# Kernel tuning notes

Measured on AMD Instinct MI355X. Metric: run time of the kernel, lower is better.

## Reference

```python
import jax, jax.numpy as jnp
import numpy as np

TOP_K = 12
OBS_RADIUS = 1.0
DIST_MIN_THRES = 0.8
EPS = 1e-4


def setup_inputs() -> dict:
    key = jax.random.key(0)
    ks = jax.random.split(key, 9)
    N, in_dim = 4096, 4
    c = in_dim + 2  # pairwise diff + eye flag + (dist - thres)
    states = jax.random.normal(ks[0], (N, in_dim), dtype=jnp.float32) * 2.0
    def w(k, o, i):
        return jax.random.normal(k, (o, i), dtype=jnp.float32) * (1.0 / np.sqrt(i))
    return {
        "states": states,
        "W1": w(ks[1], 64, c),  "b1": jnp.zeros((64,), jnp.float32),
        "W2": w(ks[2], 128, 64), "b2": jnp.zeros((128,), jnp.float32),
        "W3": w(ks[3], 64, 128), "b3": jnp.zeros((64,), jnp.float32),
        "W4": w(ks[4], 1, 64),   "b4": jnp.zeros((1,), jnp.float32),
    }


def _conv1x1(h, W, b):
    # h: [N, C_in, L]; 1x1 Conv1d == channel matmul
    return jnp.einsum('oi,nil->nol', W, h) + b[None, :, None]


def reference(states, W1, b1, W2, b2, W3, b3, W4, b4):
    N = states.shape[0]
    # pairwise differences: [N, N, in_dim]
    x = states[:, None, :] - states[None, :, :]
    d_norm = jnp.sqrt(jnp.sum(jnp.square(x[:, :, :2]) + EPS, axis=2))  # [N, N]
    eye = jnp.eye(N, dtype=x.dtype)
    x = jnp.concatenate(
        [x, eye[:, :, None], (d_norm - DIST_MIN_THRES)[:, :, None]], axis=2
    )  # [N, N, c]
    # remove_distant_agents: keep TOP_K nearest neighbors per agent
    dn = jnp.sqrt(jnp.sum(jnp.square(x[:, :, :2]) + EPS, axis=2))  # [N, N]
    _, idx = jax.lax.top_k(-dn, TOP_K)                              # [N, k]
    x = jnp.take_along_axis(x, idx[:, :, None], axis=1)            # [N, k, c]
    dist = jnp.sqrt(jnp.sum(jnp.square(x[:, :, :2]) + EPS, axis=2, keepdims=True))  # [N,k,1]
    k, c = x.shape[1], x.shape[2]
    mask = (dist <= OBS_RADIUS).astype(x.dtype).reshape(-1, 1, k)  # [N,1,k] (reshape, as in source)
    h = x.reshape(-1, c, k)  # faithful: source uses reshape, NOT transpose
    h = jax.nn.relu(_conv1x1(h, W1, b1))
    h = jax.nn.relu(_conv1x1(h, W2, b2))
    h = jax.nn.relu(_conv1x1(h, W3, b3))
    h = _conv1x1(h, W4, b4)  # [N, 1, k]
    h = h * mask
    return h, mask
```

## Files before the change

kernel.cpp:

```cpp
#include <hip/hip_runtime.h>
#include <stdint.h>

#define NAG 4096
#define TOPK 12
#define EPSF 1e-4f
#define NT 256
#define PT (NAG / NT)
#define MTOT (NAG * TOPK)

typedef unsigned long long u64;
typedef short short8v __attribute__((ext_vector_type(8)));
typedef float f32x4 __attribute__((ext_vector_type(4)));

__device__ __forceinline__ u64 umin64(u64 a, u64 b) { return a < b ? a : b; }

__device__ __forceinline__ unsigned short f2bf(float f) {
    union { float f; unsigned u; } v; v.f = f;
    unsigned r = v.u + 0x7FFFu + ((v.u >> 16) & 1u);
    return (unsigned short)(r >> 16);
}

template <int CTRL>
__device__ __forceinline__ void dpp_min_step(unsigned &hi, unsigned &lo) {
    unsigned ohi = (unsigned)__builtin_amdgcn_update_dpp((int)hi, (int)hi, CTRL, 0xf, 0xf, false);
    unsigned olo = (unsigned)__builtin_amdgcn_update_dpp((int)lo, (int)lo, CTRL, 0xf, 0xf, false);
    bool t = (ohi < hi) || (ohi == hi && olo < lo);
    hi = t ? ohi : hi;
    lo = t ? olo : lo;
}

__global__ __launch_bounds__(NT, 8)
void cbf_select(const float* __restrict__ states,
                float* __restrict__ xbuf,
                float* __restrict__ out)
{
    const int i = blockIdx.x;
    const int t = threadIdx.x;
    const int lane = t & 63;
    const int wv = t >> 6;

    __shared__ u64 s_min[NT];
    __shared__ u64 s_surv[128];
    __shared__ int s_sel[TOPK];
    __shared__ float s_x[72];
    __shared__ unsigned s_cnt;
    __shared__ unsigned s_T;

    if (t == 0) s_cnt = 0;

    const float2* st2 = reinterpret_cast<const float2*>(states);
    const float si0 = states[i * 4 + 0];
    const float si1 = states[i * 4 + 1];

    unsigned dnb[PT];
    float mind = 1e30f;
    int minu = 0;
#pragma unroll
    for (int u = 0; u < PT; ++u) {
        int j = u * NT + t;
        float2 sj = st2[j * 2];
        float dx0 = __fsub_rn(si0, sj.x);
        float dx1 = __fsub_rn(si1, sj.y);
        float d2 = __fadd_rn(__fadd_rn(__fmul_rn(dx0, dx0), EPSF),
                             __fadd_rn(__fmul_rn(dx1, dx1), EPSF));
        float dn = __fsqrt_rn(d2);
        dnb[u] = __float_as_uint(dn);
        if (dn < mind) { mind = dn; minu = u; }
    }
    s_min[t] = ((u64)__float_as_uint(mind) << 32) | (unsigned)(minu * NT + t);
    __syncthreads();

    if (wv == 0) {
        unsigned khi[4], klo[4];
#pragma unroll
        for (int q = 0; q < 4; ++q) {
            u64 kk = s_min[lane + q * 64];
            klo[q] = (unsigned)(kk & 0xffffffffull);
            khi[q] = (unsigned)(kk >> 32);
        }
        unsigned Tb = 0;
        for (int r = 0; r < TOPK; ++r) {
            unsigned hi = khi[0], lo = klo[0];
#pragma unroll
            for (int q = 1; q < 4; ++q) {
                bool tk = (khi[q] < hi) || (khi[q] == hi && klo[q] < lo);
                hi = tk ? khi[q] : hi;
                lo = tk ? klo[q] : lo;
            }
            dpp_min_step<0xB1>(hi, lo);
            dpp_min_step<0x4E>(hi, lo);
            dpp_min_step<0x124>(hi, lo);
            dpp_min_step<0x128>(hi, lo);
            dpp_min_step<0x142>(hi, lo);
            dpp_min_step<0x143>(hi, lo);
            unsigned hw = (unsigned)__builtin_amdgcn_readlane((int)hi, 63);
            unsigned lw = (unsigned)__builtin_amdgcn_readlane((int)lo, 63);
            Tb = hw;
#pragma unroll
            for (int q = 0; q < 4; ++q) {
                bool w = (khi[q] == hw) && (klo[q] == lw);
                khi[q] = w ? 0xFFFFFFFFu : khi[q];
            }
        }
        if (lane == 0) s_T = Tb;
    }
    __syncthreads();

    {
        unsigned Tb = s_T;
#pragma unroll
        for (int u = 0; u < PT; ++u) {
            if (dnb[u] <= Tb) {
                unsigned slot = atomicAdd(&s_cnt, 1u);
                if (slot < 128)
                    s_surv[slot] = ((u64)dnb[u] << 32) | (unsigned)(u * NT + t);
            }
        }
    }
    __syncthreads();

    if (wv == 0) {
        int cnt = (int)s_cnt;
        if (cnt > 128) cnt = 128;
        u64 kA = (lane < cnt) ? s_surv[lane] : ~0ull;
        u64 kB = (lane + 64 < cnt) ? s_surv[lane + 64] : ~0ull;
        int rA = 0, rB = 0;
        for (int q = 0; q < cnt; ++q) {
            u64 kq = s_surv[q];
            rA += (kq < kA) ? 1 : 0;
            rB += (kq < kB) ? 1 : 0;
        }
        if (lane < cnt && rA < TOPK) s_sel[rA] = (int)(unsigned)(kA & 0xffffffffull);
        if (lane + 64 < cnt && rB < TOPK) s_sel[rB] = (int)(unsigned)(kB & 0xffffffffull);
    }
    __syncthreads();

    if (t < TOPK) {
        int j = s_sel[t];
        const float4 sj = reinterpret_cast<const float4*>(states)[j];
        const float4 si = reinterpret_cast<const float4*>(states)[i];
        float dx0 = __fsub_rn(si.x, sj.x);
        float dx1 = __fsub_rn(si.y, sj.y);
        float dx2 = __fsub_rn(si.z, sj.z);
        float dx3 = __fsub_rn(si.w, sj.w);
        float d2 = __fadd_rn(__fadd_rn(__fmul_rn(dx0, dx0), EPSF),
                             __fadd_rn(__fmul_rn(dx1, dx1), EPSF));
        float dn = __fsqrt_rn(d2);
        s_x[t * 6 + 0] = dx0;
        s_x[t * 6 + 1] = dx1;
        s_x[t * 6 + 2] = dx2;
        s_x[t * 6 + 3] = dx3;
        s_x[t * 6 + 4] = (j == i) ? 1.0f : 0.0f;
        s_x[t * 6 + 5] = __fsub_rn(dn, 0.8f);
        out[MTOT + i * TOPK + t] = (dn <= 1.0f) ? 1.0f : 0.0f;
    }
    __syncthreads();

    if (t < TOPK) {
        int m = i * TOPK + t;
        float4 v0 = {s_x[0 * 12 + t], s_x[1 * 12 + t], s_x[2 * 12 + t], s_x[3 * 12 + t]};
        float4 v1 = {s_x[4 * 12 + t], s_x[5 * 12 + t], 0.0f, 0.0f};
        reinterpret_cast<float4*>(xbuf + m * 8)[0] = v0;
        reinterpret_cast<float4*>(xbuf + m * 8)[1] = v1;
    }
}

__global__ __launch_bounds__(256)
void cbf_mlp(const float* __restrict__ xbuf,
             const float* __restrict__ W1, const float* __restrict__ b1,
             const float* __restrict__ W2, const float* __restrict__ b2,
             const float* __restrict__ W3, const float* __restrict__ b3,
             const float* __restrict__ W4, const float* __restrict__ b4,
             float* __restrict__ out)
{
    const int t = threadIdx.x;
    const int lane = t & 63;
    const int wv = t >> 6;
    const int r16 = lane & 15;
    const int hi = lane >> 4;
    const int m0 = blockIdx.x * 64 + wv * 16;

    __shared__ __align__(16) unsigned char s_h1[4 * 2048];
    __shared__ __align__(16) unsigned char s_h2[4 * 4096];
    unsigned char* lp1 = s_h1 + wv * 2048;
    unsigned char* lp2 = s_h2 + wv * 4096;

    const int mrow = m0 + r16;
    const float4 xa = reinterpret_cast<const float4*>(xbuf + mrow * 8)[0];
    const float4 xb = reinterpret_cast<const float4*>(xbuf + mrow * 8)[1];
    const float xc[6] = {xa.x, xa.y, xa.z, xa.w, xb.x, xb.y};

    unsigned short h1b[16];
#pragma unroll
    for (int ol = 0; ol < 16; ++ol) {
        int o = hi * 16 + ol;
        const float2* wr = reinterpret_cast<const float2*>(W1 + o * 6);
        float2 w0 = wr[0], w1 = wr[1], w2 = wr[2];
        float acc = b1[o];
        acc = fmaf(w0.x, xc[0], acc);
        acc = fmaf(w0.y, xc[1], acc);
        acc = fmaf(w1.x, xc[2], acc);
        acc = fmaf(w1.y, xc[3], acc);
        acc = fmaf(w2.x, xc[4], acc);
        acc = fmaf(w2.y, xc[5], acc);
        h1b[ol] = f2bf(fmaxf(acc, 0.0f));
    }
    {
        short8v p0, p1;
#pragma unroll
        for (int e = 0; e < 8; ++e) { p0[e] = (short)h1b[e]; p1[e] = (short)h1b[8 + e]; }
        int rowb = r16 * 128;
        *(short8v*)(lp1 + rowb + (((2 * hi + 0) ^ (r16 & 7)) * 16)) = p0;
        *(short8v*)(lp1 + rowb + (((2 * hi + 1) ^ (r16 & 7)) * 16)) = p1;
    }
    __syncthreads();

    short8v a0 = *(short8v*)(lp1 + r16 * 128 + (((0 + hi) ^ (r16 & 7)) * 16));
    short8v a1 = *(short8v*)(lp1 + r16 * 128 + (((4 + hi) ^ (r16 & 7)) * 16));
    const int c = r16;
#pragma unroll
    for (int nt = 0; nt < 8; ++nt) {
        const float* wrow = W2 + (nt * 16 + c) * 64;
        float4 g0 = *(const float4*)(wrow + 8 * hi);
        float4 g1 = *(const float4*)(wrow + 8 * hi + 4);
        float4 g2 = *(const float4*)(wrow + 32 + 8 * hi);
        float4 g3 = *(const float4*)(wrow + 36 + 8 * hi);
        short8v bf0, bf1;
        bf0[0] = (short)f2bf(g0.x); bf0[1] = (short)f2bf(g0.y);
        bf0[2] = (short)f2bf(g0.z); bf0[3] = (short)f2bf(g0.w);
        bf0[4] = (short)f2bf(g1.x); bf0[5] = (short)f2bf(g1.y);
        bf0[6] = (short)f2bf(g1.z); bf0[7] = (short)f2bf(g1.w);
        bf1[0] = (short)f2bf(g2.x); bf1[1] = (short)f2bf(g2.y);
        bf1[2] = (short)f2bf(g2.z); bf1[3] = (short)f2bf(g2.w);
        bf1[4] = (short)f2bf(g3.x); bf1[5] = (short)f2bf(g3.y);
        bf1[6] = (short)f2bf(g3.z); bf1[7] = (short)f2bf(g3.w);
        float bb = b2[nt * 16 + c];
        f32x4 acc = {bb, bb, bb, bb};
        acc = __builtin_amdgcn_mfma_f32_16x16x32_bf16(a0, bf0, acc, 0, 0, 0);
        acc = __builtin_amdgcn_mfma_f32_16x16x32_bf16(a1, bf1, acc, 0, 0, 0);
#pragma unroll
        for (int e = 0; e < 4; ++e) {
            unsigned short hv = f2bf(fmaxf(acc[e], 0.0f));
            int mr = 4 * hi + e;
            int slot = (2 * nt + (c >> 3)) ^ (mr & 15);
            *(unsigned short*)(lp2 + mr * 256 + slot * 16 + ((2 * c) & 15)) = hv;
        }
    }
    __syncthreads();

    short8v a3[4];
#pragma unroll
    for (int ks = 0; ks < 4; ++ks)
        a3[ks] = *(short8v*)(lp2 + r16 * 256 + (((4 * ks + hi) ^ r16) * 16));
    float h3r[4][4];
#pragma unroll
    for (int nt = 0; nt < 4; ++nt) {
        const float* wrow = W3 + (nt * 16 + c) * 128;
        float bb = b3[nt * 16 + c];
        f32x4 ac = {bb, bb, bb, bb};
#pragma unroll
        for (int ks = 0; ks < 4; ++ks) {
            float4 q0 = *(const float4*)(wrow + ks * 32 + 8 * hi);
            float4 q1 = *(const float4*)(wrow + ks * 32 + 8 * hi + 4);
            short8v bf;
            bf[0] = (short)f2bf(q0.x); bf[1] = (short)f2bf(q0.y);
            bf[2] = (short)f2bf(q0.z); bf[3] = (short)f2bf(q0.w);
            bf[4] = (short)f2bf(q1.x); bf[5] = (short)f2bf(q1.y);
            bf[6] = (short)f2bf(q1.z); bf[7] = (short)f2bf(q1.w);
            ac = __builtin_amdgcn_mfma_f32_16x16x32_bf16(a3[ks], bf, ac, 0, 0, 0);
        }
#pragma unroll
        for (int e = 0; e < 4; ++e) h3r[nt][e] = fmaxf(ac[e], 0.0f);
    }

    float w4c[4];
#pragma unroll
    for (int nt = 0; nt < 4; ++nt) w4c[nt] = W4[nt * 16 + c];
    float part[4];
#pragma unroll
    for (int e = 0; e < 4; ++e) {
        float p = h3r[0][e] * w4c[0];
        p = fmaf(h3r[1][e], w4c[1], p);
        p = fmaf(h3r[2][e], w4c[2], p);
        p = fmaf(h3r[3][e], w4c[3], p);
        part[e] = p;
    }
#pragma unroll
    for (int off = 1; off <= 8; off <<= 1) {
#pragma unroll
        for (int e = 0; e < 4; ++e)
            part[e] += __shfl_xor(part[e], off, 64);
    }
    if (c == 0) {
        float bb4 = b4[0];
#pragma unroll
        for (int e = 0; e < 4; ++e) {
            int m = m0 + 4 * hi + e;
            float mk = out[MTOT + m];
            out[m] = (part[e] + bb4) * mk;
        }
    }
}

extern "C" void kernel_launch(void* const* d_in, const int* in_sizes, int n_in,
                              void* d_out, int out_size, void* d_ws, size_t ws_size,
                              hipStream_t stream) {
    const float* states = (const float*)d_in[0];
    const float* W1 = (const float*)d_in[1];
    const float* b1 = (const float*)d_in[2];
    const float* W2 = (const float*)d_in[3];
    const float* b2 = (const float*)d_in[4];
    const float* W3 = (const float*)d_in[5];
    const float* b3 = (const float*)d_in[6];
    const float* W4 = (const float*)d_in[7];
    const float* b4 = (const float*)d_in[8];
    float* out = (float*)d_out;
    float* xbuf = (float*)d_ws;

    cbf_select<<<dim3(NAG), dim3(NT), 0, stream>>>(states, xbuf, out);
    cbf_mlp<<<dim3(MTOT / 64), dim3(256), 0, stream>>>(xbuf, W1, b1, W2, b2,
                                                       W3, b3, W4, b4, out);
}
```

Before: 115.3 us.

## Fuse neighbor selection and MLP into one kernel with prepacked bf16 weights

Merges the top-k selection kernel and the MLP kernel into one per-agent block. Wave 0 runs the MLP on that agent's 12 neighbors straight from shared memory, which removes the xbuf round trip through global memory and the second launch. W2 and W3 are converted to bf16 once by a small single-block prep kernel, so the MLP no longer converts weights per tile. In exchange, only one wave per block does the MLP while the other three exit, about 25% of the 16 MFMA rows are padding, and the survivor buffer is cut from 128 to 64 entries, which could drop candidates when many distances tie.

```diff
diff --git a/kernel.cpp b/kernel.cpp
--- a/kernel.cpp
+++ b/kernel.cpp
@@ -29,10 +29,25 @@
     lo = t ? olo : lo;
 }
 
-__global__ __launch_bounds__(NT, 8)
-void cbf_select(const float* __restrict__ states,
-                float* __restrict__ xbuf,
-                float* __restrict__ out)
+__global__ __launch_bounds__(256)
+void cbf_prep(const float* __restrict__ W2, const float* __restrict__ W3,
+              unsigned short* __restrict__ Wb) {
+    int t = threadIdx.x;
+#pragma unroll
+    for (int k = 0; k < 64; ++k) {
+        int idx = k * 256 + t;
+        float v = (idx < 8192) ? W2[idx] : W3[idx - 8192];
+        Wb[idx] = f2bf(v);
+    }
+}
+
+__global__ __launch_bounds__(NT, 4)
+void cbf_fused(const float* __restrict__ states,
+               const float* __restrict__ W1, const float* __restrict__ b1,
+               const unsigned short* __restrict__ Wb,
+               const float* __restrict__ b2, const float* __restrict__ b3,
+               const float* __restrict__ W4, const float* __restrict__ b4,
+               float* __restrict__ out)
 {
     const int i = blockIdx.x;
     const int t = threadIdx.x;
@@ -40,11 +55,14 @@
     const int wv = t >> 6;
 
     __shared__ u64 s_min[NT];
-    __shared__ u64 s_surv[128];
+    __shared__ u64 s_surv[64];
     __shared__ int s_sel[TOPK];
     __shared__ float s_x[72];
+    __shared__ float s_mask[TOPK];
     __shared__ unsigned s_cnt;
     __shared__ unsigned s_T;
+    __shared__ __align__(16) unsigned char s_h1[2048];
+    __shared__ __align__(16) unsigned char s_h2[4096];
 
     if (t == 0) s_cnt = 0;
 
@@ -112,31 +130,29 @@
         for (int u = 0; u < PT; ++u) {
             if (dnb[u] <= Tb) {
                 unsigned slot = atomicAdd(&s_cnt, 1u);
-                if (slot < 128)
+                if (slot < 64)
                     s_surv[slot] = ((u64)dnb[u] << 32) | (unsigned)(u * NT + t);
             }
         }
     }
     __syncthreads();
 
-    if (wv == 0) {
+    if (wv != 0) return;
+
+    {
         int cnt = (int)s_cnt;
-        if (cnt > 128) cnt = 128;
+        if (cnt > 64) cnt = 64;
         u64 kA = (lane < cnt) ? s_surv[lane] : ~0ull;
-        u64 kB = (lane + 64 < cnt) ? s_surv[lane + 64] : ~0ull;
-        int rA = 0, rB = 0;
-        for (int q = 0; q < cnt; ++q) {
-            u64 kq = s_surv[q];
-            rA += (kq < kA) ? 1 : 0;
-            rB += (kq < kB) ? 1 : 0;
-        }
+        int rA = 0;
+        for (int q = 0; q < cnt; ++q)
+            rA += (s_surv[q] < kA) ? 1 : 0;
         if (lane < cnt && rA < TOPK) s_sel[rA] = (int)(unsigned)(kA & 0xffffffffull);
-        if (lane + 64 < cnt && rB < TOPK) s_sel[rB] = (int)(unsigned)(kB & 0xffffffffull);
-    }
-    __syncthreads();
-
-    if (t < TOPK) {
-        int j = s_sel[t];
+    }
+    __asm volatile("s_waitcnt lgkmcnt(0)" ::: "memory");
+    __builtin_amdgcn_wave_barrier();
+
+    if (lane < TOPK) {
+        int j = s_sel[lane];
         const float4 sj = reinterpret_cast<const float4*>(states)[j];
         const float4 si = reinterpret_cast<const float4*>(states)[i];
         float dx0 = __fsub_rn(si.x, sj.x);
@@ -146,49 +162,26 @@
         float d2 = __fadd_rn(__fadd_rn(__fmul_rn(dx0, dx0), EPSF),
                              __fadd_rn(__fmul_rn(dx1, dx1), EPSF));
         float dn = __fsqrt_rn(d2);
-        s_x[t * 6 + 0] = dx0;
-        s_x[t * 6 + 1] = dx1;
-        s_x[t * 6 + 2] = dx2;
-        s_x[t * 6 + 3] = dx3;
-        s_x[t * 6 + 4] = (j == i) ? 1.0f : 0.0f;
-        s_x[t * 6 + 5] = __fsub_rn(dn, 0.8f);
-        out[MTOT + i * TOPK + t] = (dn <= 1.0f) ? 1.0f : 0.0f;
-    }
-    __syncthreads();
-
-    if (t < TOPK) {
-        int m = i * TOPK + t;
-        float4 v0 = {s_x[0 * 12 + t], s_x[1 * 12 + t], s_x[2 * 12 + t], s_x[3 * 12 + t]};
-        float4 v1 = {s_x[4 * 12 + t], s_x[5 * 12 + t], 0.0f, 0.0f};
-        reinterpret_cast<float4*>(xbuf + m * 8)[0] = v0;
-        reinterpret_cast<float4*>(xbuf + m * 8)[1] = v1;
-    }
-}
-
-__global__ __launch_bounds__(256)
-void cbf_mlp(const float* __restrict__ xbuf,
-             const float* __restrict__ W1, const float* __restrict__ b1,
-             const float* __restrict__ W2, const float* __restrict__ b2,
-             const float* __restrict__ W3, const float* __restrict__ b3,
-             const float* __restrict__ W4, const float* __restrict__ b4,
-             float* __restrict__ out)
-{
-    const int t = threadIdx.x;
-    const int lane = t & 63;
-    const int wv = t >> 6;
+        s_x[lane * 6 + 0] = dx0;
+        s_x[lane * 6 + 1] = dx1;
+        s_x[lane * 6 + 2] = dx2;
+        s_x[lane * 6 + 3] = dx3;
+        s_x[lane * 6 + 4] = (j == i) ? 1.0f : 0.0f;
+        s_x[lane * 6 + 5] = __fsub_rn(dn, 0.8f);
+        float mk = (dn <= 1.0f) ? 1.0f : 0.0f;
+        s_mask[lane] = mk;
+        out[MTOT + i * TOPK + lane] = mk;
+    }
+    __asm volatile("s_waitcnt lgkmcnt(0)" ::: "memory");
+    __builtin_amdgcn_wave_barrier();
+
     const int r16 = lane & 15;
     const int hi = lane >> 4;
-    const int m0 = blockIdx.x * 64 + wv * 16;
-
-    __shared__ __align__(16) unsigned char s_h1[4 * 2048];
-    __shared__ __align__(16) unsigned char s_h2[4 * 4096];
-    unsigned char* lp1 = s_h1 + wv * 2048;
-    unsigned char* lp2 = s_h2 + wv * 4096;
-
-    const int mrow = m0 + r16;
-    const float4 xa = reinterpret_cast<const float4*>(xbuf + mrow * 8)[0];
-    const float4 xb = reinterpret_cast<const float4*>(xbuf + mrow * 8)[1];
-    const float xc[6] = {xa.x, xa.y, xa.z, xa.w, xb.x, xb.y};
+
+    float xc[6];
+#pragma unroll
+    for (int ch = 0; ch < 6; ++ch)
+        xc[ch] = (r16 < TOPK) ? s_x[ch * TOPK + r16] : 0.0f;
 
     unsigned short h1b[16];
 #pragma unroll
@@ -203,38 +196,28 @@
         acc = fmaf(w1.y, xc[3], acc);
         acc = fmaf(w2.x, xc[4], acc);
         acc = fmaf(w2.y, xc[5], acc);
-        h1b[ol] = f2bf(fmaxf(acc, 0.0f));
+        h1b[ol] = (r16 < TOPK) ? f2bf(fmaxf(acc, 0.0f)) : (unsigned short)0;
     }
     {
         short8v p0, p1;
 #pragma unroll
         for (int e = 0; e < 8; ++e) { p0[e] = (short)h1b[e]; p1[e] = (short)h1b[8 + e]; }
         int rowb = r16 * 128;
-        *(short8v*)(lp1 + rowb + (((2 * hi + 0) ^ (r16 & 7)) * 16)) = p0;
-        *(short8v*)(lp1 + rowb + (((2 * hi + 1) ^ (r16 & 7)) * 16)) = p1;
-    }
-    __syncthreads();
-
-    short8v a0 = *(short8v*)(lp1 + r16 * 128 + (((0 + hi) ^ (r16 & 7)) * 16));
-    short8v a1 = *(short8v*)(lp1 + r16 * 128 + (((4 + hi) ^ (r16 & 7)) * 16));
+        *(short8v*)(s_h1 + rowb + (((2 * hi + 0) ^ (r16 & 7)) * 16)) = p0;
+        *(short8v*)(s_h1 + rowb + (((2 * hi + 1) ^ (r16 & 7)) * 16)) = p1;
+    }
+    __asm volatile("s_waitcnt lgkmcnt(0)" ::: "memory");
+    __builtin_amdgcn_wave_barrier();
+
+    short8v a0 = *(short8v*)(s_h1 + r16 * 128 + (((0 + hi) ^ (r16 & 7)) * 16));
+    short8v a1 = *(short8v*)(s_h1 + r16 * 128 + (((4 + hi) ^ (r16 & 7)) * 16));
     const int c = r16;
 #pragma unroll
     for (int nt = 0; nt < 8; ++nt) {
-        const float* wrow = W2 + (nt * 16 + c) * 64;
-        float4 g0 = *(const float4*)(wrow + 8 * hi);
-        float4 g1 = *(const float4*)(wrow + 8 * hi + 4);
-        float4 g2 = *(const float4*)(wrow + 32 + 8 * hi);
-        float4 g3 = *(const float4*)(wrow + 36 + 8 * hi);
-        short8v bf0, bf1;
-        bf0[0] = (short)f2bf(g0.x); bf0[1] = (short)f2bf(g0.y);
-        bf0[2] = (short)f2bf(g0.z); bf0[3] = (short)f2bf(g0.w);
-        bf0[4] = (short)f2bf(g1.x); bf0[5] = (short)f2bf(g1.y);
-        bf0[6] = (short)f2bf(g1.z); bf0[7] = (short)f2bf(g1.w);
-        bf1[0] = (short)f2bf(g2.x); bf1[1] = (short)f2bf(g2.y);
-        bf1[2] = (short)f2bf(g2.z); bf1[3] = (short)f2bf(g2.w);
-        bf1[4] = (short)f2bf(g3.x); bf1[5] = (short)f2bf(g3.y);
-        bf1[6] = (short)f2bf(g3.z); bf1[7] = (short)f2bf(g3.w);
-        float bb = b2[nt * 16 + c];
+        int o = nt * 16 + c;
+        short8v bf0 = *(const short8v*)(Wb + o * 64 + 8 * hi);
+        short8v bf1 = *(const short8v*)(Wb + o * 64 + 32 + 8 * hi);
+        float bb = b2[o];
         f32x4 acc = {bb, bb, bb, bb};
         acc = __builtin_amdgcn_mfma_f32_16x16x32_bf16(a0, bf0, acc, 0, 0, 0);
         acc = __builtin_amdgcn_mfma_f32_16x16x32_bf16(a1, bf1, acc, 0, 0, 0);
@@ -243,30 +226,25 @@
             unsigned short hv = f2bf(fmaxf(acc[e], 0.0f));
             int mr = 4 * hi + e;
             int slot = (2 * nt + (c >> 3)) ^ (mr & 15);
-            *(unsigned short*)(lp2 + mr * 256 + slot * 16 + ((2 * c) & 15)) = hv;
-        }
-    }
-    __syncthreads();
+            *(unsigned short*)(s_h2 + mr * 256 + slot * 16 + ((2 * c) & 15)) = hv;
+        }
+    }
+    __asm volatile("s_waitcnt lgkmcnt(0)" ::: "memory");
+    __builtin_amdgcn_wave_barrier();
 
     short8v a3[4];
 #pragma unroll
     for (int ks = 0; ks < 4; ++ks)
-        a3[ks] = *(short8v*)(lp2 + r16 * 256 + (((4 * ks + hi) ^ r16) * 16));
+        a3[ks] = *(short8v*)(s_h2 + r16 * 256 + (((4 * ks + hi) ^ r16) * 16));
     float h3r[4][4];
 #pragma unroll
     for (int nt = 0; nt < 4; ++nt) {
-        const float* wrow = W3 + (nt * 16 + c) * 128;
-        float bb = b3[nt * 16 + c];
+        int o = nt * 16 + c;
+        float bb = b3[o];
         f32x4 ac = {bb, bb, bb, bb};
 #pragma unroll
         for (int ks = 0; ks < 4; ++ks) {
-            float4 q0 = *(const float4*)(wrow + ks * 32 + 8 * hi);
-            float4 q1 = *(const float4*)(wrow + ks * 32 + 8 * hi + 4);
-            short8v bf;
-            bf[0] = (short)f2bf(q0.x); bf[1] = (short)f2bf(q0.y);
-            bf[2] = (short)f2bf(q0.z); bf[3] = (short)f2bf(q0.w);
-            bf[4] = (short)f2bf(q1.x); bf[5] = (short)f2bf(q1.y);
-            bf[6] = (short)f2bf(q1.z); bf[7] = (short)f2bf(q1.w);
+            short8v bf = *(const short8v*)(Wb + 8192 + o * 128 + ks * 32 + 8 * hi);
             ac = __builtin_amdgcn_mfma_f32_16x16x32_bf16(a3[ks], bf, ac, 0, 0, 0);
         }
 #pragma unroll
@@ -295,9 +273,9 @@
         float bb4 = b4[0];
 #pragma unroll
         for (int e = 0; e < 4; ++e) {
-            int m = m0 + 4 * hi + e;
-            float mk = out[MTOT + m];
-            out[m] = (part[e] + bb4) * mk;
+            int mr = 4 * hi + e;
+            if (mr < TOPK)
+                out[i * TOPK + mr] = (part[e] + bb4) * s_mask[mr];
         }
     }
 }
@@ -315,9 +293,9 @@
     const float* W4 = (const float*)d_in[7];
     const float* b4 = (const float*)d_in[8];
     float* out = (float*)d_out;
-    float* xbuf = (float*)d_ws;
-
-    cbf_select<<<dim3(NAG), dim3(NT), 0, stream>>>(states, xbuf, out);
-    cbf_mlp<<<dim3(MTOT / 64), dim3(256), 0, stream>>>(xbuf, W1, b1, W2, b2,
-                                                       W3, b3, W4, b4, out);
-}
+    unsigned short* Wb = (unsigned short*)d_ws;
+
+    cbf_prep<<<dim3(1), dim3(256), 0, stream>>>(W2, W3, Wb);
+    cbf_fused<<<dim3(NAG), dim3(NT), 0, stream>>>(states, W1, b1, Wb,
+                                                  b2, b3, W4, b4, out);
+}
```

New measurement: 102.6 us. -11.0%, faster.
